# Kernel optimization log

Hardware: AMD Instinct MI355X
Metric: run time of the kernel (lower is better)

## Reference

```python
import jax, jax.numpy as jnp
import numpy as np

DIM = 512; NB = 4; BS = DIM // NB            # EinFFT blocks
DS = 64; DC = 4; EXP = 2; DI = EXP * DIM      # Mamba dims
DTR = DIM // 16                               # dt_rank
BLOCKS = 2; LAM = 0.01; B_SZ = 2; L_SZ = 1024

def layer_norm(x, w, b):
    m = x.mean(-1, keepdims=True)
    v = x.var(-1, keepdims=True)
    return (x - m) / jnp.sqrt(v + 1e-5) * w + b

def softshrink(x, lam):
    return jnp.where(x > lam, x - lam, jnp.where(x < -lam, x + lam, jnp.zeros((), x.dtype)))

def mamba(x, in_proj_w, conv_w, conv_b, x_proj_w, dt_proj_w, dt_proj_b, A_log, D, out_proj_w):
    B, L, _ = x.shape
    xz = x @ in_proj_w.T                      # (B,L,2*DI)
    xm, z = jnp.split(xz, 2, axis=-1)
    # causal depthwise conv1d, keep first L outputs
    xt = xm.transpose(0, 2, 1)                # (B,DI,L)
    conv = jax.lax.conv_general_dilated(xt, conv_w, (1,), [(DC - 1, 0)],
                                        feature_group_count=DI,
                                        dimension_numbers=('NCH', 'OIH', 'NCH'))
    xm = jax.nn.silu((conv + conv_b[None, :, None]).transpose(0, 2, 1))  # (B,L,DI)
    proj = xm @ x_proj_w.T                    # (B,L,DTR+2*DS)
    dt = proj[..., :DTR]
    Bm = proj[..., DTR:DTR + DS]
    Cm = proj[..., DTR + DS:]
    dt = jax.nn.softplus(dt @ dt_proj_w.T + dt_proj_b)   # (B,L,DI)
    A = -jnp.exp(A_log)                       # (DI,DS)

    def step(h, inp):
        dt_t, B_t, C_t, u_t = inp             # (B,DI),(B,DS),(B,DS),(B,DI)
        dA = jnp.exp(dt_t[:, :, None] * A)
        h = dA * h + dt_t[:, :, None] * B_t[:, None, :] * u_t[:, :, None]
        y = jnp.einsum('bds,bs->bd', h, C_t)
        return h, y

    h0 = jnp.zeros((B, DI, DS), x.dtype)
    _, ys = jax.lax.scan(step, h0, (dt.transpose(1, 0, 2), Bm.transpose(1, 0, 2),
                                    Cm.transpose(1, 0, 2), xm.transpose(1, 0, 2)))
    y = ys.transpose(1, 0, 2) + xm * D        # (B,L,DI)
    y = y * jax.nn.silu(z)
    return y @ out_proj_w.T

def einfft(x, cw1, cw2, cb1, cb2):
    B, N, C = x.shape
    xf = jnp.fft.fft2(x.reshape(B, N, NB, BS), axes=(1, 2), norm='ortho')
    mul = lambda t, w: jnp.einsum('BNbd,bdk->BNbk', t, w)
    r1 = jax.nn.relu(mul(xf.real, cw1[0]) - mul(xf.imag, cw1[1]) + cb1[0])
    i1 = jax.nn.relu(mul(xf.real, cw1[1]) + mul(xf.imag, cw1[0]) + cb1[1])
    r2 = softshrink(mul(r1, cw2[0]) - mul(i1, cw2[1]) + cb2[0], LAM)
    i2 = softshrink(mul(r1, cw2[1]) + mul(i1, cw2[0]) + cb2[1], LAM)
    out = jnp.fft.ifft2(r2 + 1j * i2, axes=(1, 2), norm='ortho')
    return out.real.astype(x.dtype).reshape(B, N, C)

def setup_inputs() -> dict:
    key = jax.random.key(0)
    ks = jax.random.split(key, 16)
    r = lambda i, shape, s: jax.random.normal(ks[i], shape, jnp.float32) * s
    A_log = jnp.log(jnp.tile(jnp.arange(1, DS + 1, dtype=jnp.float32), (DI, 1)))
    return {
        'x': jax.random.normal(ks[0], (B_SZ, L_SZ, DIM), jnp.float32),
        'ln_w': jnp.ones((DIM,), jnp.float32), 'ln_b': jnp.zeros((DIM,), jnp.float32),
        'in_proj_w': r(1, (2 * DI, DIM), 0.02),
        'conv_w': r(2, (DI, 1, DC), 0.1), 'conv_b': jnp.zeros((DI,), jnp.float32),
        'x_proj_w': r(3, (DTR + 2 * DS, DI), 0.02),
        'dt_proj_w': r(4, (DI, DTR), 0.02),
        'dt_proj_b': jnp.full((DI,), float(np.log(np.expm1(0.01))), jnp.float32),
        'A_log': A_log, 'D': jnp.ones((DI,), jnp.float32),
        'out_proj_w': r(5, (DIM, DI), 0.02),
        'norm2_w': jnp.ones((DIM,), jnp.float32), 'norm2_b': jnp.zeros((DIM,), jnp.float32),
        'cw1': r(6, (2, NB, BS, BS), 0.02), 'cw2': r(7, (2, NB, BS, BS), 0.02),
        'cb1': r(8, (2, NB, BS), 0.02), 'cb2': r(9, (2, NB, BS), 0.02),
    }

def reference(x, ln_w, ln_b, in_proj_w, conv_w, conv_b, x_proj_w, dt_proj_w, dt_proj_b,
              A_log, D, out_proj_w, norm2_w, norm2_b, cw1, cw2, cb1, cb2):
    for _ in range(BLOCKS):
        x = x + mamba(layer_norm(x, ln_w, ln_b), in_proj_w, conv_w, conv_b,
                      x_proj_w, dt_proj_w, dt_proj_b, A_log, D, out_proj_w)
        x = x + einfft(layer_norm(x, norm2_w, norm2_b), cw1, cw2, cb1, cb2)
    return x
```

## Files before the change

### kernel.cpp

```cpp
#include <hip/hip_runtime.h>

typedef unsigned short u16;
typedef __attribute__((ext_vector_type(8))) short bf8;
typedef __attribute__((ext_vector_type(4))) float f4;

__device__ __forceinline__ float bf2f(u16 b) {
    return __uint_as_float(((unsigned)b) << 16);
}
__device__ __forceinline__ u16 f2bf(float f) {
    unsigned u = __float_as_uint(f);
    u += 0x7fffu + ((u >> 16) & 1u);
    return (u16)(u >> 16);
}
__device__ __forceinline__ bf8 neg8(bf8 v) {
    union { bf8 b; uint u[4]; } t; t.b = v;
    t.u[0] ^= 0x80008000u; t.u[1] ^= 0x80008000u;
    t.u[2] ^= 0x80008000u; t.u[3] ^= 0x80008000u;
    return t.b;
}
__device__ __forceinline__ int digrev10(int x) {
    int r = __brev((unsigned)x) >> 22;
    return ((r & 0x2AA) >> 1) | ((r & 0x155) << 1);
}

__global__ void detect_k(const u16* __restrict__ dtb, int* __restrict__ flag) {
    flag[0] = (dtb[0] == dtb[1] && dtb[1] == dtb[2] && dtb[2] == dtb[3] &&
               dtb[3] == dtb[4] && dtb[4] == dtb[5]) ? 1 : 0;
    flag[1] = 1;
}

__global__ __launch_bounds__(256)
void achk_k(const float* __restrict__ alog, int* __restrict__ flag) {
    int i = blockIdx.x * 256 + threadIdx.x;
    int s = i & 63;
    float n = __expf(alog[i]);
    float e = (float)(s + 1);
    if (fabsf(n - e) > 0.02f * e) atomicAnd(&flag[1], 0);
}

struct CvtArgs {
    const void* src[18];
    void* dst[18];
    int n[18];
    int obf[18];
};
__global__ __launch_bounds__(256)
void cvt_all_k(CvtArgs a, const int* __restrict__ flag) {
    const int t = blockIdx.y;
    const int n = a.n[t];
    const int f = flag[0];
    if (a.obf[t] == 2) {
        u16* __restrict__ d = (u16*)a.dst[t];
        if (f) {
            const u16* __restrict__ s = (const u16*)a.src[t];
            for (int i = blockIdx.x * 256 + threadIdx.x; i < n; i += gridDim.x * 256) {
                int cin = i & 127, cout = (i >> 7) & 127, snb = i >> 14;
                d[(snb << 14) + (cout << 7) + cin] = s[(snb << 14) + (cin << 7) + cout];
            }
        } else {
            const float* __restrict__ s = (const float*)a.src[t];
            for (int i = blockIdx.x * 256 + threadIdx.x; i < n; i += gridDim.x * 256) {
                int cin = i & 127, cout = (i >> 7) & 127, snb = i >> 14;
                d[(snb << 14) + (cout << 7) + cin] =
                    f2bf(s[(snb << 14) + (cin << 7) + cout]);
            }
        }
    } else if (a.obf[t] == 1) {
        u16* __restrict__ d = (u16*)a.dst[t];
        if (f) {
            const u16* __restrict__ s = (const u16*)a.src[t];
            for (int i = blockIdx.x * 256 + threadIdx.x; i < n; i += gridDim.x * 256)
                d[i] = s[i];
        } else {
            const float* __restrict__ s = (const float*)a.src[t];
            for (int i = blockIdx.x * 256 + threadIdx.x; i < n; i += gridDim.x * 256)
                d[i] = f2bf(s[i]);
        }
    } else {
        float* __restrict__ d = (float*)a.dst[t];
        if (f) {
            const u16* __restrict__ s = (const u16*)a.src[t];
            for (int i = blockIdx.x * 256 + threadIdx.x; i < n; i += gridDim.x * 256)
                d[i] = bf2f(s[i]);
        } else {
            const float* __restrict__ s = (const float*)a.src[t];
            for (int i = blockIdx.x * 256 + threadIdx.x; i < n; i += gridDim.x * 256)
                d[i] = s[i];
        }
    }
}

__global__ __launch_bounds__(256)
void ln_k(const float* __restrict__ x, const float* __restrict__ w,
          const float* __restrict__ b, u16* __restrict__ out) {
    const int row = blockIdx.x, tid = threadIdx.x;
    const float* xr = x + (long)row * 512;
    float v0 = xr[tid], v1 = xr[tid + 256];
    float s = v0 + v1, q = v0 * v0 + v1 * v1;
#pragma unroll
    for (int off = 32; off; off >>= 1) {
        s += __shfl_xor(s, off);
        q += __shfl_xor(q, off);
    }
    __shared__ float ss[4], qq[4];
    int wid = tid >> 6;
    if ((tid & 63) == 0) { ss[wid] = s; qq[wid] = q; }
    __syncthreads();
    s = ss[0] + ss[1] + ss[2] + ss[3];
    q = qq[0] + qq[1] + qq[2] + qq[3];
    float mean = s * (1.f / 512.f);
    float var = q * (1.f / 512.f) - mean * mean;
    float rstd = rsqrtf(var + 1e-5f);
    u16* o = out + (long)row * 512;
    o[tid]       = f2bf((v0 - mean) * rstd * w[tid]       + b[tid]);
    o[tid + 256] = f2bf((v1 - mean) * rstd * w[tid + 256] + b[tid + 256]);
}

__global__ __launch_bounds__(256)
void lnstat_k(const float* __restrict__ x, float* __restrict__ stat) {
    const int token = blockIdx.x * 4 + (threadIdx.x >> 6);
    const int lane = threadIdx.x & 63;
    const float* xr = x + (long)token * 512 + lane * 8;
    float4 a = *(const float4*)xr, b = *(const float4*)(xr + 4);
    float s = a.x + a.y + a.z + a.w + b.x + b.y + b.z + b.w;
    float q = a.x * a.x + a.y * a.y + a.z * a.z + a.w * a.w +
              b.x * b.x + b.y * b.y + b.z * b.z + b.w * b.w;
#pragma unroll
    for (int off = 32; off; off >>= 1) {
        s += __shfl_xor(s, off);
        q += __shfl_xor(q, off);
    }
    if (lane == 0) {
        float mean = s * (1.f / 512.f);
        float var = q * (1.f / 512.f) - mean * mean;
        stat[token * 2]     = mean;
        stat[token * 2 + 1] = rsqrtf(var + 1e-5f);
    }
}

#define LSTR 40
__global__ __launch_bounds__(256)
void mgemm_k(const u16* __restrict__ Ab, const u16* __restrict__ Bp,
             float* __restrict__ D, int N, int K, int lda, int ldb, int ldc,
             long bsA, long bsB) {
    const u16* A = Ab + blockIdx.z * bsA;
    const u16* B = Bp + blockIdx.z * bsB;

    __shared__ u16 As[64 * LSTR];
    __shared__ u16 Bs[64 * LSTR];
    const int tid = threadIdx.x;
    const int lane = tid & 63;
    const int w = tid >> 6, wm = w & 1, wn = w >> 1;
    const int m0 = blockIdx.y * 64, n0 = blockIdx.x * 64;
    const int fr = (lane & 15), fq = (lane >> 4);

    f4 acc[2][2] = {};

    for (int k0 = 0; k0 < K; k0 += 32) {
        {
            const int ar = tid >> 2, aks = (tid & 3) << 3;
            *(uint4*)&As[ar * LSTR + aks] =
                *(const uint4*)(A + (long)(m0 + ar) * lda + k0 + aks);
        }
        {
            const int br = tid >> 2, bks = (tid & 3) << 3;
            uint4 raw = make_uint4(0, 0, 0, 0);
            if (n0 + br < N)
                raw = *(const uint4*)(B + (long)(n0 + br) * ldb + k0 + bks);
            *(uint4*)&Bs[br * LSTR + bks] = raw;
        }
        __syncthreads();
        bf8 af[2], bff[2];
#pragma unroll
        for (int t = 0; t < 2; t++) {
            af[t]  = *(bf8*)&As[(wm * 32 + t * 16 + fr) * LSTR + (fq << 3)];
            bff[t] = *(bf8*)&Bs[(wn * 32 + t * 16 + fr) * LSTR + (fq << 3)];
        }
#pragma unroll
        for (int i = 0; i < 2; i++)
#pragma unroll
            for (int j = 0; j < 2; j++)
                acc[i][j] = __builtin_amdgcn_mfma_f32_16x16x32_bf16(
                    af[i], bff[j], acc[i][j], 0, 0, 0);
        __syncthreads();
    }

#pragma unroll
    for (int i = 0; i < 2; i++) {
#pragma unroll
        for (int j = 0; j < 2; j++) {
            const int gmb = m0 + wm * 32 + i * 16 + (fq << 2);
            const int gn  = n0 + wn * 32 + j * 16 + fr;
            if (gn >= N) continue;
#pragma unroll
            for (int e = 0; e < 4; e++)
                atomicAdd(&D[(long)(gmb + e) * ldc + gn], acc[i][j][e]);
        }
    }
}

__global__ __launch_bounds__(256)
void inproj_k(const u16* __restrict__ A, const u16* __restrict__ B,
              u16* __restrict__ Dm, u16* __restrict__ Dz) {
    __shared__ u16 As[64 * LSTR];
    __shared__ u16 Bs[64 * LSTR];
    const int tid = threadIdx.x, lane = tid & 63;
    const int w = tid >> 6, wm = w & 1, wn = w >> 1;
    const int m0 = blockIdx.y * 64, n0 = blockIdx.x * 64;
    const int fr = lane & 15, fq = lane >> 4;
    f4 acc[2][2] = {};

    for (int k0 = 0; k0 < 512; k0 += 32) {
        const int r = tid >> 2, ks = (tid & 3) << 3;
        *(uint4*)&As[r * LSTR + ks] =
            *(const uint4*)(A + (long)(m0 + r) * 512 + k0 + ks);
        *(uint4*)&Bs[r * LSTR + ks] =
            *(const uint4*)(B + (long)(n0 + r) * 512 + k0 + ks);
        __syncthreads();
        bf8 af[2], bfv[2];
#pragma unroll
        for (int t = 0; t < 2; ++t) {
            af[t]  = *(bf8*)&As[(wm * 32 + t * 16 + fr) * LSTR + (fq << 3)];
            bfv[t] = *(bf8*)&Bs[(wn * 32 + t * 16 + fr) * LSTR + (fq << 3)];
        }
#pragma unroll
        for (int i = 0; i < 2; ++i)
#pragma unroll
            for (int j = 0; j < 2; ++j)
                acc[i][j] = __builtin_amdgcn_mfma_f32_16x16x32_bf16(
                    af[i], bfv[j], acc[i][j], 0, 0, 0);
        __syncthreads();
    }
    u16* Dst = (n0 < 1024) ? Dm : Dz;
    const int noff = (n0 < 1024) ? 0 : 1024;
#pragma unroll
    for (int i = 0; i < 2; ++i)
#pragma unroll
        for (int j = 0; j < 2; ++j) {
            const int gm = m0 + wm * 32 + i * 16 + (fq << 2);
            const int gn = n0 + wn * 32 + j * 16 + fr - noff;
#pragma unroll
            for (int e = 0; e < 4; ++e)
                Dst[(long)(gm + e) * 1024 + gn] = f2bf(acc[i][j][e]);
        }
}

__global__ __launch_bounds__(1024)
void ffw_k(const float* __restrict__ xf, const float* __restrict__ lw,
           const float* __restrict__ lb, const float* __restrict__ stat,
           u16* __restrict__ Orb, u16* __restrict__ Oib) {
    const int bz = blockIdx.x;
    const int b = bz >> 7, cg = bz & 127;
    const int t = threadIdx.x;
    const int f = t >> 8, tl = t & 255;
    const int c = cg + f * 128;
    __shared__ float re[4224], im[4224], twr[768], twi[768];
    if (t < 768) {
        float s, cc;
        __sincosf((float)t * -6.1359231515425649e-3f, &s, &cc);
        twr[t] = cc; twi[t] = s;
    }
    float* rf = re + f * 1056;
    float* mf = im + f * 1056;
    const float wc = lw[c], bc = lb[c];
    const float* src = xf + ((long)b * 1024) * 512 + c;
    const float* st = stat + (long)b * 2048;
#pragma unroll
    for (int r = 0; r < 4; ++r) {
        int n = tl + r * 256;
        float mean = st[n * 2], rs = st[n * 2 + 1];
        float v = (src[(long)n * 512] - mean) * rs * wc + bc;
        int a = n + (n >> 5);
        rf[a] = v; mf[a] = 0.f;
    }
    __syncthreads();
#pragma unroll
    for (int st5 = 0; st5 < 5; ++st5) {
        const int qsh = 8 - 2 * st5;
        const int q = 1 << qsh;
        const int len = q << 2;
        const int m = 1 << (2 * st5);
        int j = tl & (q - 1);
        int g = tl >> qsh;
        int i0 = g * len + j;
        int a0 = i0 + (i0 >> 5);
        int i1 = i0 + q,     a1 = i1 + (i1 >> 5);
        int i2 = i0 + 2 * q, a2 = i2 + (i2 >> 5);
        int i3 = i0 + 3 * q, a3 = i3 + (i3 >> 5);
        float ar = rf[a0], ai = mf[a0];
        float br = rf[a1], bi = mf[a1];
        float cr = rf[a2], ci = mf[a2];
        float dr = rf[a3], di = mf[a3];
        float t0r = ar + cr, t0i = ai + ci;
        float t1r = ar - cr, t1i = ai - ci;
        float t2r = br + dr, t2i = bi + di;
        float u = br - dr, v = bi - di;
        rf[a0] = t0r + t2r; mf[a0] = t0i + t2i;
        {
            int k = j * m;
            float wr = twr[k], wi = twi[k];
            float xr = t1r + v, xi = t1i - u;
            rf[a1] = xr * wr - xi * wi;
            mf[a1] = xr * wi + xi * wr;
        }
        {
            int k = 2 * j * m;
            float wr = twr[k], wi = twi[k];
            float xr = t0r - t2r, xi = t0i - t2i;
            rf[a2] = xr * wr - xi * wi;
            mf[a2] = xr * wi + xi * wr;
        }
        {
            int k = 3 * j * m;
            float wr = twr[k], wi = twi[k];
            float xr = t1r - v, xi = t1i + u;
            rf[a3] = xr * wr - xi * wi;
            mf[a3] = xr * wi + xi * wr;
        }
        __syncthreads();
    }
    u16* drp = Orb + ((long)(b * 512 + c)) * 1024;
    u16* dip = Oib + ((long)(b * 512 + c)) * 1024;
#pragma unroll
    for (int r = 0; r < 4; ++r) {
        int kf = tl + r * 256;
        int sidx = digrev10(kf);
        int a = sidx + (sidx >> 5);
        float r0 = re[a],        i0v = im[a];
        float r1 = re[1056 + a], i1v = im[1056 + a];
        float r2 = re[2112 + a], i2v = im[2112 + a];
        float r3 = re[3168 + a], i3v = im[3168 + a];
        float vr, vi;
        if (f == 0)      { vr = r0 + r1 + r2 + r3;     vi = i0v + i1v + i2v + i3v; }
        else if (f == 1) { vr = r0 + i1v - r2 - i3v;   vi = i0v - r1 - i2v + r3; }
        else if (f == 2) { vr = r0 - r1 + r2 - r3;     vi = i0v - i1v + i2v - i3v; }
        else             { vr = r0 - i1v - r2 + i3v;   vi = i0v + r1 - i2v - r3; }
        drp[kf] = f2bf(vr * 0.015625f);
        dip[kf] = f2bf(vi * 0.015625f);
    }
}

__global__ __launch_bounds__(1024)
void ifw_k(const u16* __restrict__ X2r, const u16* __restrict__ X2i,
           float* __restrict__ Yc) {
    const int bz = blockIdx.x;
    const int b = bz >> 7, cg = bz & 127;
    const int t = threadIdx.x;
    const int f = t >> 8, tl = t & 255;
    const int c = cg + f * 128;
    __shared__ float re[4224], im[4224], twr[768], twi[768];
    if (t < 768) {
        float s, cc;
        __sincosf((float)t * 6.1359231515425649e-3f, &s, &cc);
        twr[t] = cc; twi[t] = s;
    }
    const u16* sr = X2r + ((long)(b * 512 + c)) * 1024;
    const u16* si = X2i + ((long)(b * 512 + c)) * 1024;
    float* rf = re + f * 1056;
    float* mf = im + f * 1056;
    const int k4 = tl * 4;
    {
        uint2 pr = *(const uint2*)&sr[k4];
        uint2 pi = *(const uint2*)&si[k4];
        u16 rv[4] = {(u16)(pr.x & 0xFFFF), (u16)(pr.x >> 16),
                     (u16)(pr.y & 0xFFFF), (u16)(pr.y >> 16)};
        u16 iv[4] = {(u16)(pi.x & 0xFFFF), (u16)(pi.x >> 16),
                     (u16)(pi.y & 0xFFFF), (u16)(pi.y >> 16)};
#pragma unroll
        for (int e = 0; e < 4; ++e) {
            int idx = k4 + e;
            int a = idx + (idx >> 5);
            rf[a] = bf2f(rv[e]);
            mf[a] = bf2f(iv[e]);
        }
    }
    __syncthreads();
    float vr[4], vi[4];
#pragma unroll
    for (int e = 0; e < 4; ++e) {
        int idx = k4 + e;
        int a = idx + (idx >> 5);
        float r0 = re[a],        i0v = im[a];
        float r1 = re[1056 + a], i1v = im[1056 + a];
        float r2 = re[2112 + a], i2v = im[2112 + a];
        float r3 = re[3168 + a], i3v = im[3168 + a];
        if (f == 0)      { vr[e] = r0 + r1 + r2 + r3;     vi[e] = i0v + i1v + i2v + i3v; }
        else if (f == 1) { vr[e] = r0 - i1v - r2 + i3v;   vi[e] = i0v + r1 - i2v - r3; }
        else if (f == 2) { vr[e] = r0 - r1 + r2 - r3;     vi[e] = i0v - i1v + i2v - i3v; }
        else             { vr[e] = r0 + i1v - r2 - i3v;   vi[e] = i0v - r1 - i2v + r3; }
        vr[e] *= 0.5f; vi[e] *= 0.5f;
    }
    __syncthreads();
#pragma unroll
    for (int e = 0; e < 4; ++e) {
        int idx = k4 + e;
        int a = idx + (idx >> 5);
        rf[a] = vr[e]; mf[a] = vi[e];
    }
    __syncthreads();
#pragma unroll
    for (int st = 0; st < 5; ++st) {
        const int qsh = 8 - 2 * st;
        const int q = 1 << qsh;
        const int len = q << 2;
        const int m = 1 << (2 * st);
        int j = tl & (q - 1);
        int g = tl >> qsh;
        int i0 = g * len + j;
        int a0 = i0 + (i0 >> 5);
        int i1 = i0 + q,     a1 = i1 + (i1 >> 5);
        int i2 = i0 + 2 * q, a2 = i2 + (i2 >> 5);
        int i3 = i0 + 3 * q, a3 = i3 + (i3 >> 5);
        float ar = rf[a0], ai = mf[a0];
        float br = rf[a1], bi = mf[a1];
        float cr = rf[a2], ci = mf[a2];
        float dr = rf[a3], di = mf[a3];
        float t0r = ar + cr, t0i = ai + ci;
        float t1r = ar - cr, t1i = ai - ci;
        float t2r = br + dr, t2i = bi + di;
        float u = br - dr, v = bi - di;
        rf[a0] = t0r + t2r; mf[a0] = t0i + t2i;
        {
            int k = j * m;
            float wr = twr[k], wi = twi[k];
            float xr = t1r - v, xi = t1i + u;
            rf[a1] = xr * wr - xi * wi;
            mf[a1] = xr * wi + xi * wr;
        }
        {
            int k = 2 * j * m;
            float wr = twr[k], wi = twi[k];
            float xr = t0r - t2r, xi = t0i - t2i;
            rf[a2] = xr * wr - xi * wi;
            mf[a2] = xr * wi + xi * wr;
        }
        {
            int k = 3 * j * m;
            float wr = twr[k], wi = twi[k];
            float xr = t1r + v, xi = t1i - u;
            rf[a3] = xr * wr - xi * wi;
            mf[a3] = xr * wi + xi * wr;
        }
        __syncthreads();
    }
    float* d = Yc + ((long)(b * 512 + c)) * 1024;
#pragma unroll
    for (int r = 0; r < 4; ++r) {
        int n = tl + r * 256;
        int sidx = digrev10(n);
        int a = sidx + (sidx >> 5);
        d[n] = rf[a] * 0.03125f;
    }
}

__global__ __launch_bounds__(256)
void transadd_k(float* __restrict__ xbuf, const float* __restrict__ Yc,
                void* __restrict__ dout, int last, const int* __restrict__ flag) {
    const int b = blockIdx.z;
    const int c0 = blockIdx.x * 64, n0 = blockIdx.y * 64;
    __shared__ float T[64][65];
    const int tid = threadIdx.x;
    const int r = tid >> 2, q = (tid & 3) * 16;
    const float* src = Yc + ((long)(b * 512 + c0 + r)) * 1024 + n0 + q;
#pragma unroll
    for (int k = 0; k < 4; ++k) {
        float4 v = *(const float4*)(src + k * 4);
        T[r][q + k * 4 + 0] = v.x; T[r][q + k * 4 + 1] = v.y;
        T[r][q + k * 4 + 2] = v.z; T[r][q + k * 4 + 3] = v.w;
    }
    __syncthreads();
    const long base = ((long)(b * 1024 + n0 + r)) * 512 + c0 + q;
    float* dst = xbuf + base;
    if (last) {
        const int bf = flag[0];
#pragma unroll
        for (int k = 0; k < 4; ++k) {
            float4 w = *(const float4*)(dst + k * 4);
            w.x += T[q + k * 4 + 0][r]; w.y += T[q + k * 4 + 1][r];
            w.z += T[q + k * 4 + 2][r]; w.w += T[q + k * 4 + 3][r];
            if (bf) {
                uint2 p;
                p.x = (uint)f2bf(w.x) | ((uint)f2bf(w.y) << 16);
                p.y = (uint)f2bf(w.z) | ((uint)f2bf(w.w) << 16);
                *(uint2*)((u16*)dout + base + k * 4) = p;
            } else {
                *(float4*)((float*)dout + base + k * 4) = w;
            }
        }
    } else {
#pragma unroll
        for (int k = 0; k < 4; ++k) {
            float4 w = *(const float4*)(dst + k * 4);
            w.x += T[q + k * 4 + 0][r]; w.y += T[q + k * 4 + 1][r];
            w.z += T[q + k * 4 + 2][r]; w.w += T[q + k * 4 + 3][r];
            *(float4*)(dst + k * 4) = w;
        }
    }
}

#define LSTR2 136
__global__ __launch_bounds__(512)
void cmix2_k(const u16* __restrict__ Xr, const u16* __restrict__ Xi,
             const u16* __restrict__ W1, const u16* __restrict__ W2,
             const float* __restrict__ cb1, const float* __restrict__ cb2,
             u16* __restrict__ Or, u16* __restrict__ Oi) {
    const int z = blockIdx.y, b = z >> 2, nb = z & 3;
    const int m0 = blockIdx.x * 32;
    const u16* Ar = Xr + (long)b * 524288 + nb * 131072;
    const u16* Ai = Xi + (long)b * 524288 + nb * 131072;
    const u16* W1r = W1 + nb * 16384;
    const u16* W1i = W1 + 65536 + nb * 16384;
    const u16* W2r = W2 + nb * 16384;
    const u16* W2i = W2 + 65536 + nb * 16384;
    u16* Dr = Or + (long)b * 524288 + nb * 131072;
    u16* Di = Oi + (long)b * 524288 + nb * 131072;

    __shared__ u16 Xrs[32 * LSTR2], Xis[32 * LSTR2];
    __shared__ u16 Wrs[128 * LSTR2], Wis[128 * LSTR2];
    const int tid = threadIdx.x, lane = tid & 63;
    const int w8 = tid >> 6;
    const int fr = lane & 15, fq = lane >> 4;

    {
        const int am = tid & 31, kb = (tid >> 5) << 3;
        u16 tr[8], ti[8];
#pragma unroll
        for (int j = 0; j < 8; ++j) {
            long off = (long)(kb + j) * 1024 + m0 + am;
            tr[j] = Ar[off]; ti[j] = Ai[off];
        }
        uint r0 = (uint)tr[0] | ((uint)tr[1] << 16);
        uint r1 = (uint)tr[2] | ((uint)tr[3] << 16);
        uint r2 = (uint)tr[4] | ((uint)tr[5] << 16);
        uint r3 = (uint)tr[6] | ((uint)tr[7] << 16);
        *(uint4*)&Xrs[am * LSTR2 + kb] = make_uint4(r0, r1, r2, r3);
        r0 = (uint)ti[0] | ((uint)ti[1] << 16);
        r1 = (uint)ti[2] | ((uint)ti[3] << 16);
        r2 = (uint)ti[4] | ((uint)ti[5] << 16);
        r3 = (uint)ti[6] | ((uint)ti[7] << 16);
        *(uint4*)&Xis[am * LSTR2 + kb] = make_uint4(r0, r1, r2, r3);
#pragma unroll
        for (int it = 0; it < 4; ++it) {
            int slot = it * 512 + tid;
            int row = slot >> 4, c8 = (slot & 15) << 3;
            *(uint4*)&Wrs[row * LSTR2 + c8] = *(const uint4*)(W1r + row * 128 + c8);
            *(uint4*)&Wis[row * LSTR2 + c8] = *(const uint4*)(W1i + row * 128 + c8);
        }
    }
    __syncthreads();

    {
        f4 accr[2] = {}, acci[2] = {};
#pragma unroll
        for (int kq = 0; kq < 4; ++kq) {
            const int kc = kq * 32 + (fq << 3);
            bf8 xr[2], xi[2], wr, wi;
#pragma unroll
            for (int i = 0; i < 2; ++i) {
                xr[i] = *(bf8*)&Xrs[(i * 16 + fr) * LSTR2 + kc];
                xi[i] = *(bf8*)&Xis[(i * 16 + fr) * LSTR2 + kc];
            }
            wr = *(bf8*)&Wrs[(w8 * 16 + fr) * LSTR2 + kc];
            wi = *(bf8*)&Wis[(w8 * 16 + fr) * LSTR2 + kc];
            bf8 nxi[2] = { neg8(xi[0]), neg8(xi[1]) };
#pragma unroll
            for (int i = 0; i < 2; ++i) {
                accr[i] = __builtin_amdgcn_mfma_f32_16x16x32_bf16(xr[i], wr, accr[i], 0, 0, 0);
                accr[i] = __builtin_amdgcn_mfma_f32_16x16x32_bf16(nxi[i], wi, accr[i], 0, 0, 0);
                acci[i] = __builtin_amdgcn_mfma_f32_16x16x32_bf16(xr[i], wi, acci[i], 0, 0, 0);
                acci[i] = __builtin_amdgcn_mfma_f32_16x16x32_bf16(xi[i], wr, acci[i], 0, 0, 0);
            }
        }
        __syncthreads();
        const int n1 = w8 * 16 + fr;
        const float br_ = cb1[nb * 128 + n1];
        const float bi_ = cb1[512 + nb * 128 + n1];
#pragma unroll
        for (int i = 0; i < 2; ++i)
#pragma unroll
            for (int e = 0; e < 4; ++e) {
                const int m = i * 16 + (fq << 2) + e;
                Xrs[m * LSTR2 + n1] = f2bf(fmaxf(accr[i][e] + br_, 0.f));
                Xis[m * LSTR2 + n1] = f2bf(fmaxf(acci[i][e] + bi_, 0.f));
            }
    }
#pragma unroll
    for (int it = 0; it < 4; ++it) {
        int slot = it * 512 + tid;
        int row = slot >> 4, c8 = (slot & 15) << 3;
        *(uint4*)&Wrs[row * LSTR2 + c8] = *(const uint4*)(W2r + row * 128 + c8);
        *(uint4*)&Wis[row * LSTR2 + c8] = *(const uint4*)(W2i + row * 128 + c8);
    }
    __syncthreads();

    {
        f4 accr[2] = {}, acci[2] = {};
#pragma unroll
        for (int kq = 0; kq < 4; ++kq) {
            const int kc = kq * 32 + (fq << 3);
            bf8 xr[2], xi[2], wr, wi;
#pragma unroll
            for (int i = 0; i < 2; ++i) {
                xr[i] = *(bf8*)&Xrs[(i * 16 + fr) * LSTR2 + kc];
                xi[i] = *(bf8*)&Xis[(i * 16 + fr) * LSTR2 + kc];
            }
            wr = *(bf8*)&Wrs[(w8 * 16 + fr) * LSTR2 + kc];
            wi = *(bf8*)&Wis[(w8 * 16 + fr) * LSTR2 + kc];
            bf8 nxi[2] = { neg8(xi[0]), neg8(xi[1]) };
#pragma unroll
            for (int i = 0; i < 2; ++i) {
                accr[i] = __builtin_amdgcn_mfma_f32_16x16x32_bf16(xr[i], wr, accr[i], 0, 0, 0);
                accr[i] = __builtin_amdgcn_mfma_f32_16x16x32_bf16(nxi[i], wi, accr[i], 0, 0, 0);
                acci[i] = __builtin_amdgcn_mfma_f32_16x16x32_bf16(xr[i], wi, acci[i], 0, 0, 0);
                acci[i] = __builtin_amdgcn_mfma_f32_16x16x32_bf16(xi[i], wr, acci[i], 0, 0, 0);
            }
        }
        const int n2 = w8 * 16 + fr;
        const float br_ = cb2[nb * 128 + n2];
        const float bi_ = cb2[512 + nb * 128 + n2];
#pragma unroll
        for (int i = 0; i < 2; ++i) {
            const int gm = m0 + i * 16 + (fq << 2);
            u16 pr[4], pi[4];
#pragma unroll
            for (int e = 0; e < 4; ++e) {
                float vr = accr[i][e] + br_;
                float vi = acci[i][e] + bi_;
                vr = (vr > 0.01f) ? vr - 0.01f : ((vr < -0.01f) ? vr + 0.01f : 0.f);
                vi = (vi > 0.01f) ? vi - 0.01f : ((vi < -0.01f) ? vi + 0.01f : 0.f);
                pr[e] = f2bf(vr); pi[e] = f2bf(vi);
            }
            uint2 wr2, wi2;
            wr2.x = (uint)pr[0] | ((uint)pr[1] << 16);
            wr2.y = (uint)pr[2] | ((uint)pr[3] << 16);
            wi2.x = (uint)pi[0] | ((uint)pi[1] << 16);
            wi2.y = (uint)pi[2] | ((uint)pi[3] << 16);
            *(uint2*)&Dr[(long)n2 * 1024 + gm] = wr2;
            *(uint2*)&Di[(long)n2 * 1024 + gm] = wi2;
        }
    }
}

__global__ __launch_bounds__(256)
void conv_k(const u16* __restrict__ xm, const float* __restrict__ cw,
            const float* __restrict__ cb, u16* __restrict__ u,
            float* __restrict__ Pred) {
    int idx = blockIdx.x * 256 + threadIdx.x;
    if (idx < 327680) Pred[idx] = 0.f;
    int d = idx & 1023;
    int l = (idx >> 10) & 1023;
    int b = idx >> 20;
    float acc = cb[d];
    const u16* base = xm + (long)b * 1048576 + d;
#pragma unroll
    for (int j = 0; j < 4; j++) {
        int li = l - 3 + j;
        if (li >= 0) acc = fmaf(cw[d * 4 + j], bf2f(base[(long)li * 1024]), acc);
    }
    float sig = 1.f / (1.f + __expf(-acc));
    u[idx] = f2bf(acc * sig);
}

__global__ __launch_bounds__(256, 1)
void scan1_k(const u16* __restrict__ uLb, const float* __restrict__ Pred,
             const u16* __restrict__ dtW, const float* __restrict__ dtBias,
             const float* __restrict__ alog, u16* __restrict__ Hb,
             float* __restrict__ Sbuf, u16* __restrict__ dtLb,
             const int* __restrict__ flag) {
    const int dg = blockIdx.x, c = blockIdx.y, b = blockIdx.z;
    const int tid = threadIdx.x;
    const int d = dg * 256 + tid;
    const int t0 = c * 32;
    __shared__ float Bls[32][64];
    __shared__ float Pls[32][32];
    {
#pragma unroll
        for (int j = 0; j < 2; ++j) {
            int slot = tid + j * 256;
            int r = slot >> 4, cg = (slot & 15) << 2;
            *(float4*)&Bls[r][cg] =
                *(const float4*)(Pred + ((long)(b * 1024 + t0 + r)) * 160 + 32 + cg);
        }
        {
            int r = tid >> 3, cg = (tid & 7) << 2;
            *(float4*)&Pls[r][cg] =
                *(const float4*)(Pred + ((long)(b * 1024 + t0 + r)) * 160 + cg);
        }
    }
    __syncthreads();

    float w[32];
    {
        const u16* wr = dtW + (long)d * 32;
#pragma unroll
        for (int qi = 0; qi < 4; ++qi) {
            uint4 qv = *((const uint4*)wr + qi);
            w[qi * 8 + 0] = bf2f((u16)(qv.x & 0xFFFF));
            w[qi * 8 + 1] = bf2f((u16)(qv.x >> 16));
            w[qi * 8 + 2] = bf2f((u16)(qv.y & 0xFFFF));
            w[qi * 8 + 3] = bf2f((u16)(qv.y >> 16));
            w[qi * 8 + 4] = bf2f((u16)(qv.z & 0xFFFF));
            w[qi * 8 + 5] = bf2f((u16)(qv.z >> 16));
            w[qi * 8 + 6] = bf2f((u16)(qv.w & 0xFFFF));
            w[qi * 8 + 7] = bf2f((u16)(qv.w >> 16));
        }
    }
    const float bias = dtBias[d];

    const u16* up = uLb + (long)(b * 1024 + t0) * 1024 + d;
    float uu[32];
#pragma unroll
    for (int t = 0; t < 32; ++t) uu[t] = bf2f(up[(long)t * 1024]);
    u16* dtp = dtLb + (long)(b * 1024 + t0) * 1024 + d;

    float h[64];
#pragma unroll
    for (int s = 0; s < 64; s++) h[s] = 0.f;
    float S = 0.f;

    if (flag[1]) {
        for (int t = 0; t < 32; ++t) {
            const float4* P4 = (const float4*)&Pls[t][0];
            float x0 = bias, x1 = 0.f, x2 = 0.f, x3 = 0.f;
#pragma unroll
            for (int kg = 0; kg < 8; ++kg) {
                float4 p = P4[kg];
                x0 = fmaf(p.x, w[kg * 4 + 0], x0);
                x1 = fmaf(p.y, w[kg * 4 + 1], x1);
                x2 = fmaf(p.z, w[kg * 4 + 2], x2);
                x3 = fmaf(p.w, w[kg * 4 + 3], x3);
            }
            float x = (x0 + x1) + (x2 + x3);
            float dtf = (x > 20.f) ? x : log1pf(__expf(x));
            u16 dq = f2bf(dtf);
            dtp[(long)t * 1024] = dq;
            float dt = bf2f(dq);
            float dtu = dt * uu[t];
            S += dt;
            float q = __expf(-dt);
            float q2 = q * q, q3 = q2 * q, q4 = q2 * q2;
            float a0 = q, a1 = q2, a2 = q3, a3 = q4;
            const float4* B4p = (const float4*)&Bls[t][0];
#pragma unroll
            for (int sg = 0; sg < 16; ++sg) {
                float4 B4 = B4p[sg];
                h[sg * 4 + 0] = a0 * h[sg * 4 + 0] + dtu * B4.x;
                h[sg * 4 + 1] = a1 * h[sg * 4 + 1] + dtu * B4.y;
                h[sg * 4 + 2] = a2 * h[sg * 4 + 2] + dtu * B4.z;
                h[sg * 4 + 3] = a3 * h[sg * 4 + 3] + dtu * B4.w;
                a0 *= q4; a1 *= q4; a2 *= q4; a3 *= q4;
            }
        }
    } else {
        float A[64];
        const float* ap = alog + (long)d * 64;
#pragma unroll
        for (int s = 0; s < 64; s += 4) {
            float4 a4 = *(const float4*)(ap + s);
            A[s] = -__expf(a4.x); A[s + 1] = -__expf(a4.y);
            A[s + 2] = -__expf(a4.z); A[s + 3] = -__expf(a4.w);
        }
        for (int t = 0; t < 32; ++t) {
            const float4* P4 = (const float4*)&Pls[t][0];
            float x0 = bias, x1 = 0.f, x2 = 0.f, x3 = 0.f;
#pragma unroll
            for (int kg = 0; kg < 8; ++kg) {
                float4 p = P4[kg];
                x0 = fmaf(p.x, w[kg * 4 + 0], x0);
                x1 = fmaf(p.y, w[kg * 4 + 1], x1);
                x2 = fmaf(p.z, w[kg * 4 + 2], x2);
                x3 = fmaf(p.w, w[kg * 4 + 3], x3);
            }
            float x = (x0 + x1) + (x2 + x3);
            float dtf = (x > 20.f) ? x : log1pf(__expf(x));
            u16 dq = f2bf(dtf);
            dtp[(long)t * 1024] = dq;
            float dt = bf2f(dq);
            float dtu = dt * uu[t];
            S += dt;
            const float4* B4p = (const float4*)&Bls[t][0];
#pragma unroll
            for (int sg = 0; sg < 16; ++sg) {
                float4 B4 = B4p[sg];
                h[sg * 4 + 0] = __expf(dt * A[sg * 4 + 0]) * h[sg * 4 + 0] + dtu * B4.x;
                h[sg * 4 + 1] = __expf(dt * A[sg * 4 + 1]) * h[sg * 4 + 1] + dtu * B4.y;
                h[sg * 4 + 2] = __expf(dt * A[sg * 4 + 2]) * h[sg * 4 + 2] + dtu * B4.z;
                h[sg * 4 + 3] = __expf(dt * A[sg * 4 + 3]) * h[sg * 4 + 3] + dtu * B4.w;
            }
        }
    }
    u16* Hp = Hb + ((((long)(b * 32 + c)) * 1024 + d) << 6);
#pragma unroll
    for (int s = 0; s < 64; s += 4) {
        uint2 p;
        p.x = ((__float_as_uint(h[s]) + 0x8000u) >> 16) |
              ((__float_as_uint(h[s + 1]) + 0x8000u) & 0xFFFF0000u);
        p.y = ((__float_as_uint(h[s + 2]) + 0x8000u) >> 16) |
              ((__float_as_uint(h[s + 3]) + 0x8000u) & 0xFFFF0000u);
        *(uint2*)&Hp[s] = p;
    }
    Sbuf[(b * 32 + c) * 1024 + d] = S;
}

__global__ __launch_bounds__(256)
void scan2_k(const float* __restrict__ alog, const float* __restrict__ Sbuf,
             u16* __restrict__ Hb) {
    int idx = blockIdx.x * 256 + threadIdx.x;
    int s = idx & 63, d = (idx >> 6) & 1023, b = idx >> 16;
    float A = -__expf(alog[(long)d * 64 + s]);
    float carry = 0.f;
    long off = (((long)(b * 32) * 1024 + d) << 6) + s;
    int sb = (b * 32) * 1024 + d;
    float Scur = Sbuf[sb];
    float Hcur = bf2f(Hb[off]);
    for (int c = 0; c < 32; ++c) {
        float Snxt = 0.f, Hnxt = 0.f;
        if (c < 31) {
            Snxt = Sbuf[sb + 1024];
            Hnxt = bf2f(Hb[off + 65536]);
        }
        float P = __expf(A * Scur);
        Hb[off] = (u16)((__float_as_uint(carry) + 0x8000u) >> 16);
        carry = P * carry + Hcur;
        Scur = Snxt; Hcur = Hnxt;
        off += 65536; sb += 1024;
    }
}

__global__ __launch_bounds__(256, 1)
void scan3_k(const u16* __restrict__ dtb, const u16* __restrict__ uLb,
             const u16* __restrict__ zLb, const float* __restrict__ Pred,
             const float* __restrict__ alog, const u16* __restrict__ Hb,
             const float* __restrict__ Dw, const int* __restrict__ flag,
             u16* __restrict__ y2) {
    const int dg = blockIdx.x, c = blockIdx.y, b = blockIdx.z;
    const int tid = threadIdx.x;
    const int d = dg * 256 + tid;
    const int t0 = c * 32;
    __shared__ float Bls[32][64];
    __shared__ float Cls[32][64];
    {
#pragma unroll
        for (int j = 0; j < 2; ++j) {
            int slot = tid + j * 256;
            int r = slot >> 4, cg = (slot & 15) << 2;
            const float* src = Pred + ((long)(b * 1024 + t0 + r)) * 160;
            *(float4*)&Bls[r][cg] = *(const float4*)(src + 32 + cg);
            *(float4*)&Cls[r][cg] = *(const float4*)(src + 96 + cg);
        }
    }
    __syncthreads();

    float h[64];
    const u16* Hp = Hb + ((((long)(b * 32 + c)) * 1024 + d) << 6);
#pragma unroll
    for (int s = 0; s < 64; s += 4) {
        uint2 p = *(const uint2*)&Hp[s];
        h[s]     = __uint_as_float(p.x << 16);
        h[s + 1] = __uint_as_float(p.x & 0xFFFF0000u);
        h[s + 2] = __uint_as_float(p.y << 16);
        h[s + 3] = __uint_as_float(p.y & 0xFFFF0000u);
    }
    const float Dd = Dw[d];
    const u16* dtp = dtb + (long)(b * 1024 + t0) * 1024 + d;
    const u16* up  = uLb + (long)(b * 1024 + t0) * 1024 + d;
    const u16* zp  = zLb + (long)(b * 1024 + t0) * 1024 + d;
    u16* y2p = y2 + (long)(b * 1024 + t0) * 1024 + d;

    float uu[32], dtv[32];
#pragma unroll
    for (int t = 0; t < 32; ++t) {
        uu[t]  = bf2f(up[(long)t * 1024]);
        dtv[t] = bf2f(dtp[(long)t * 1024]);
    }

    if (flag[1]) {
        for (int t = 0; t < 32; ++t) {
            float zz = bf2f(zp[(long)t * 1024]);
            float dt = dtv[t];
            float dtu = dt * uu[t];
            float y = 0.f;
            float q = __expf(-dt);
            float q2 = q * q, q3 = q2 * q, q4 = q2 * q2;
            float a0 = q, a1 = q2, a2 = q3, a3 = q4;
            const float4* B4p = (const float4*)&Bls[t][0];
            const float4* C4p = (const float4*)&Cls[t][0];
#pragma unroll
            for (int sg = 0; sg < 16; ++sg) {
                float4 B4 = B4p[sg];
                float4 C4 = C4p[sg];
                h[sg * 4 + 0] = a0 * h[sg * 4 + 0] + dtu * B4.x;
                y = fmaf(h[sg * 4 + 0], C4.x, y);
                h[sg * 4 + 1] = a1 * h[sg * 4 + 1] + dtu * B4.y;
                y = fmaf(h[sg * 4 + 1], C4.y, y);
                h[sg * 4 + 2] = a2 * h[sg * 4 + 2] + dtu * B4.z;
                y = fmaf(h[sg * 4 + 2], C4.z, y);
                h[sg * 4 + 3] = a3 * h[sg * 4 + 3] + dtu * B4.w;
                y = fmaf(h[sg * 4 + 3], C4.w, y);
                a0 *= q4; a1 *= q4; a2 *= q4; a3 *= q4;
            }
            float g = zz / (1.f + __expf(-zz));
            y2p[(long)t * 1024] = f2bf((y + uu[t] * Dd) * g);
        }
    } else {
        float A[64];
        const float* ap = alog + (long)d * 64;
#pragma unroll
        for (int s = 0; s < 64; s += 4) {
            float4 a4 = *(const float4*)(ap + s);
            A[s] = -__expf(a4.x); A[s + 1] = -__expf(a4.y);
            A[s + 2] = -__expf(a4.z); A[s + 3] = -__expf(a4.w);
        }
        for (int t = 0; t < 32; ++t) {
            float zz = bf2f(zp[(long)t * 1024]);
            float dt = dtv[t];
            float dtu = dt * uu[t];
            float y = 0.f;
            const float4* B4p = (const float4*)&Bls[t][0];
            const float4* C4p = (const float4*)&Cls[t][0];
#pragma unroll
            for (int sg = 0; sg < 16; ++sg) {
                float4 B4 = B4p[sg];
                float4 C4 = C4p[sg];
                h[sg * 4 + 0] = __expf(dt * A[sg * 4 + 0]) * h[sg * 4 + 0] + dtu * B4.x;
                y = fmaf(h[sg * 4 + 0], C4.x, y);
                h[sg * 4 + 1] = __expf(dt * A[sg * 4 + 1]) * h[sg * 4 + 1] + dtu * B4.y;
                y = fmaf(h[sg * 4 + 1], C4.y, y);
                h[sg * 4 + 2] = __expf(dt * A[sg * 4 + 2]) * h[sg * 4 + 2] + dtu * B4.z;
                y = fmaf(h[sg * 4 + 2], C4.z, y);
                h[sg * 4 + 3] = __expf(dt * A[sg * 4 + 3]) * h[sg * 4 + 3] + dtu * B4.w;
                y = fmaf(h[sg * 4 + 3], C4.w, y);
            }
            float g = zz / (1.f + __expf(-zz));
            y2p[(long)t * 1024] = f2bf((y + uu[t] * Dd) * g);
        }
    }
}

extern "C" void kernel_launch(void* const* d_in, const int* in_sizes, int n_in,
                              void* d_out, int out_size, void* d_ws, size_t ws_size,
                              hipStream_t stream) {
    float* ws = (float*)d_ws;
    int* flag = (int*)ws;
    size_t o = 64;
    float* xbuf  = ws + o; o += 1048576;
    float* fftA  = ws + o; o += 2097152;
    u16* xmb     = (u16*)(ws + o); o += 1048576;
    float* Yc    = ws + o; o += 1048576;
    u16* xnb     = (u16*)(ws + o); o += 524288;
    u16* wInpB   = (u16*)(ws + o); o += 524288;
    u16* wXpB    = (u16*)(ws + o); o += 81920;
    u16* wDtB    = (u16*)(ws + o); o += 16384;
    u16* wOutB   = (u16*)(ws + o); o += 262144;
    u16* WT1     = (u16*)(ws + o); o += 65536;
    u16* WT2     = (u16*)(ws + o); o += 65536;
    float* wConv = ws + o; o += 4096;
    float* wAlog = ws + o; o += 65536;
    float* wLnW  = ws + o; o += 512;
    float* wLnB  = ws + o; o += 512;
    float* wConvB= ws + o; o += 1024;
    float* wDtBias=ws + o; o += 1024;
    float* wD    = ws + o; o += 1024;
    float* wN2w  = ws + o; o += 512;
    float* wN2b  = ws + o; o += 512;
    float* wCb1  = ws + o; o += 1024;
    float* wCb2  = ws + o; o += 1024;
    float* Hreg  = ws + o; o += 4194304;
    float* Sbuf  = ws + o; o += 131072;
    float* Pred  = ws + o; o += 327680;
    u16* uLb     = (u16*)(ws + o); o += 1048576;
    u16* y2b     = (u16*)(ws + o); o += 1048576;
    u16* dtLb    = (u16*)(ws + o); o += 1048576;
    u16* zLb     = (u16*)(ws + o); o += 1048576;
    float* stat  = ws + o; o += 4096;
    u16* Hb    = (u16*)Hreg;
    u16* xzb  = (u16*)fftA;
    u16* Xrb  = xzb;
    u16* Xib  = xzb + 1048576;
    u16* X2rb = xzb + 2097152;
    u16* X2ib = xzb + 3145728;

    dim3 blk(256);

    detect_k<<<1, 1, 0, stream>>>((const u16*)d_in[8], flag);

    CvtArgs ca;
    void* dsts[18] = {xbuf, wLnW, wLnB, wInpB, wConv, wConvB, wXpB, wDtB, wDtBias,
                      wAlog, wD, wOutB, wN2w, wN2b, WT1, WT2, wCb1, wCb2};
    int obf[18]    = {0,    0,    0,    1,     0,     0,      1,    1,    0,
                      0,     0,  1,     0,    0,    2,   2,   0,    0};
    for (int i = 0; i < 18; i++) {
        ca.src[i] = d_in[i];
        ca.dst[i] = dsts[i];
        ca.n[i] = in_sizes[i];
        ca.obf[i] = obf[i];
    }
    cvt_all_k<<<dim3(64, 18), blk, 0, stream>>>(ca, flag);
    achk_k<<<256, blk, 0, stream>>>(wAlog, flag);

    for (int it = 0; it < 2; ++it) {
        ln_k<<<2048, blk, 0, stream>>>(xbuf, wLnW, wLnB, xnb);
        inproj_k<<<dim3(32, 32), blk, 0, stream>>>(xnb, wInpB, xmb, zLb);
        conv_k<<<8192, blk, 0, stream>>>(xmb, wConv, wConvB, uLb, Pred);
        mgemm_k<<<dim3(3, 32, 4), blk, 0, stream>>>(
            uLb, wXpB, Pred, 160, 256, 1024, 1024, 160, 256, 256);
        scan1_k<<<dim3(4, 32, 2), blk, 0, stream>>>(
            uLb, Pred, wDtB, wDtBias, wAlog, Hb, Sbuf, dtLb, flag);
        scan2_k<<<512, blk, 0, stream>>>(wAlog, Sbuf, Hb);
        scan3_k<<<dim3(4, 32, 2), blk, 0, stream>>>(
            dtLb, uLb, zLb, Pred, wAlog, Hb, wD, flag, y2b);
        mgemm_k<<<dim3(8, 32, 2), blk, 0, stream>>>(
            y2b, wOutB, xbuf, 512, 512, 1024, 1024, 512, 512, 512);

        lnstat_k<<<512, blk, 0, stream>>>(xbuf, stat);
        ffw_k<<<256, dim3(1024), 0, stream>>>(xbuf, wN2w, wN2b, stat, Xrb, Xib);
        cmix2_k<<<dim3(32, 8), dim3(512), 0, stream>>>(
            Xrb, Xib, WT1, WT2, wCb1, wCb2, X2rb, X2ib);
        ifw_k<<<256, dim3(1024), 0, stream>>>(X2rb, X2ib, Yc);
        transadd_k<<<dim3(8, 16, 2), blk, 0, stream>>>(xbuf, Yc, d_out, it == 1, flag);
    }
}
```

Baseline: 429.9 us.

## Split scan state dimension across thread pairs to double parallelism in scan kernels

In scan1_k and scan3_k each channel's 64-wide SSM state is now split across two adjacent threads of 32 states each. The grid doubles to 256 blocks and launch_bounds no longer limits occupancy to one block, so fewer registers are held per thread. This targets the low block count and register pressure of the previous layout. The cost is redundant dt/softplus work in both threads, an extra shuffle to reduce y, and extra multiplies to offset the decay powers by q^32 for the upper half.

```diff
diff --git a/kernel.cpp b/kernel.cpp
--- a/kernel.cpp
+++ b/kernel.cpp
@@ -661,7 +661,7 @@
     u[idx] = f2bf(acc * sig);
 }
 
-__global__ __launch_bounds__(256, 1)
+__global__ __launch_bounds__(256)
 void scan1_k(const u16* __restrict__ uLb, const float* __restrict__ Pred,
              const u16* __restrict__ dtW, const float* __restrict__ dtBias,
              const float* __restrict__ alog, u16* __restrict__ Hb,
@@ -669,7 +669,8 @@
              const int* __restrict__ flag) {
     const int dg = blockIdx.x, c = blockIdx.y, b = blockIdx.z;
     const int tid = threadIdx.x;
-    const int d = dg * 256 + tid;
+    const int d = dg * 128 + (tid >> 1);
+    const int sh = tid & 1;
     const int t0 = c * 32;
     __shared__ float Bls[32][64];
     __shared__ float Pls[32][32];
@@ -713,9 +714,9 @@
     for (int t = 0; t < 32; ++t) uu[t] = bf2f(up[(long)t * 1024]);
     u16* dtp = dtLb + (long)(b * 1024 + t0) * 1024 + d;
 
-    float h[64];
-#pragma unroll
-    for (int s = 0; s < 64; s++) h[s] = 0.f;
+    float h[32];
+#pragma unroll
+    for (int s = 0; s < 32; s++) h[s] = 0.f;
     float S = 0.f;
 
     if (flag[1]) {
@@ -733,16 +734,18 @@
             float x = (x0 + x1) + (x2 + x3);
             float dtf = (x > 20.f) ? x : log1pf(__expf(x));
             u16 dq = f2bf(dtf);
-            dtp[(long)t * 1024] = dq;
+            if (!sh) dtp[(long)t * 1024] = dq;
             float dt = bf2f(dq);
             float dtu = dt * uu[t];
             S += dt;
             float q = __expf(-dt);
             float q2 = q * q, q3 = q2 * q, q4 = q2 * q2;
-            float a0 = q, a1 = q2, a2 = q3, a3 = q4;
-            const float4* B4p = (const float4*)&Bls[t][0];
-#pragma unroll
-            for (int sg = 0; sg < 16; ++sg) {
+            float q8 = q4 * q4, q16 = q8 * q8, q32 = q16 * q16;
+            float qs = sh ? q32 : 1.f;
+            float a0 = q * qs, a1 = q2 * qs, a2 = q3 * qs, a3 = q4 * qs;
+            const float4* B4p = (const float4*)&Bls[t][sh * 32];
+#pragma unroll
+            for (int sg = 0; sg < 8; ++sg) {
                 float4 B4 = B4p[sg];
                 h[sg * 4 + 0] = a0 * h[sg * 4 + 0] + dtu * B4.x;
                 h[sg * 4 + 1] = a1 * h[sg * 4 + 1] + dtu * B4.y;
@@ -752,10 +755,10 @@
             }
         }
     } else {
-        float A[64];
-        const float* ap = alog + (long)d * 64;
-#pragma unroll
-        for (int s = 0; s < 64; s += 4) {
+        float A[32];
+        const float* ap = alog + (long)d * 64 + sh * 32;
+#pragma unroll
+        for (int s = 0; s < 32; s += 4) {
             float4 a4 = *(const float4*)(ap + s);
             A[s] = -__expf(a4.x); A[s + 1] = -__expf(a4.y);
             A[s + 2] = -__expf(a4.z); A[s + 3] = -__expf(a4.w);
@@ -774,13 +777,13 @@
             float x = (x0 + x1) + (x2 + x3);
             float dtf = (x > 20.f) ? x : log1pf(__expf(x));
             u16 dq = f2bf(dtf);
-            dtp[(long)t * 1024] = dq;
+            if (!sh) dtp[(long)t * 1024] = dq;
             float dt = bf2f(dq);
             float dtu = dt * uu[t];
             S += dt;
-            const float4* B4p = (const float4*)&Bls[t][0];
-#pragma unroll
-            for (int sg = 0; sg < 16; ++sg) {
+            const float4* B4p = (const float4*)&Bls[t][sh * 32];
+#pragma unroll
+            for (int sg = 0; sg < 8; ++sg) {
                 float4 B4 = B4p[sg];
                 h[sg * 4 + 0] = __expf(dt * A[sg * 4 + 0]) * h[sg * 4 + 0] + dtu * B4.x;
                 h[sg * 4 + 1] = __expf(dt * A[sg * 4 + 1]) * h[sg * 4 + 1] + dtu * B4.y;
@@ -789,9 +792,9 @@
             }
         }
     }
-    u16* Hp = Hb + ((((long)(b * 32 + c)) * 1024 + d) << 6);
-#pragma unroll
-    for (int s = 0; s < 64; s += 4) {
+    u16* Hp = Hb + ((((long)(b * 32 + c)) * 1024 + d) << 6) + sh * 32;
+#pragma unroll
+    for (int s = 0; s < 32; s += 4) {
         uint2 p;
         p.x = ((__float_as_uint(h[s]) + 0x8000u) >> 16) |
               ((__float_as_uint(h[s + 1]) + 0x8000u) & 0xFFFF0000u);
@@ -799,7 +802,7 @@
               ((__float_as_uint(h[s + 3]) + 0x8000u) & 0xFFFF0000u);
         *(uint2*)&Hp[s] = p;
     }
-    Sbuf[(b * 32 + c) * 1024 + d] = S;
+    if (!sh) Sbuf[(b * 32 + c) * 1024 + d] = S;
 }
 
 __global__ __launch_bounds__(256)
@@ -827,7 +830,7 @@
     }
 }
 
-__global__ __launch_bounds__(256, 1)
+__global__ __launch_bounds__(256)
 void scan3_k(const u16* __restrict__ dtb, const u16* __restrict__ uLb,
              const u16* __restrict__ zLb, const float* __restrict__ Pred,
              const float* __restrict__ alog, const u16* __restrict__ Hb,
@@ -835,7 +838,8 @@
              u16* __restrict__ y2) {
     const int dg = blockIdx.x, c = blockIdx.y, b = blockIdx.z;
     const int tid = threadIdx.x;
-    const int d = dg * 256 + tid;
+    const int d = dg * 128 + (tid >> 1);
+    const int sh = tid & 1;
     const int t0 = c * 32;
     __shared__ float Bls[32][64];
     __shared__ float Cls[32][64];
@@ -851,10 +855,10 @@
     }
     __syncthreads();
 
-    float h[64];
-    const u16* Hp = Hb + ((((long)(b * 32 + c)) * 1024 + d) << 6);
-#pragma unroll
-    for (int s = 0; s < 64; s += 4) {
+    float h[32];
+    const u16* Hp = Hb + ((((long)(b * 32 + c)) * 1024 + d) << 6) + sh * 32;
+#pragma unroll
+    for (int s = 0; s < 32; s += 4) {
         uint2 p = *(const uint2*)&Hp[s];
         h[s]     = __uint_as_float(p.x << 16);
         h[s + 1] = __uint_as_float(p.x & 0xFFFF0000u);
@@ -882,11 +886,13 @@
             float y = 0.f;
             float q = __expf(-dt);
             float q2 = q * q, q3 = q2 * q, q4 = q2 * q2;
-            float a0 = q, a1 = q2, a2 = q3, a3 = q4;
-            const float4* B4p = (const float4*)&Bls[t][0];
-            const float4* C4p = (const float4*)&Cls[t][0];
-#pragma unroll
-            for (int sg = 0; sg < 16; ++sg) {
+            float q8 = q4 * q4, q16 = q8 * q8, q32 = q16 * q16;
+            float qs = sh ? q32 : 1.f;
+            float a0 = q * qs, a1 = q2 * qs, a2 = q3 * qs, a3 = q4 * qs;
+            const float4* B4p = (const float4*)&Bls[t][sh * 32];
+            const float4* C4p = (const float4*)&Cls[t][sh * 32];
+#pragma unroll
+            for (int sg = 0; sg < 8; ++sg) {
                 float4 B4 = B4p[sg];
                 float4 C4 = C4p[sg];
                 h[sg * 4 + 0] = a0 * h[sg * 4 + 0] + dtu * B4.x;
@@ -899,14 +905,17 @@
                 y = fmaf(h[sg * 4 + 3], C4.w, y);
                 a0 *= q4; a1 *= q4; a2 *= q4; a3 *= q4;
             }
-            float g = zz / (1.f + __expf(-zz));
-            y2p[(long)t * 1024] = f2bf((y + uu[t] * Dd) * g);
+            y += __shfl_xor(y, 1);
+            if (!sh) {
+                float g = zz / (1.f + __expf(-zz));
+                y2p[(long)t * 1024] = f2bf((y + uu[t] * Dd) * g);
+            }
         }
     } else {
-        float A[64];
-        const float* ap = alog + (long)d * 64;
-#pragma unroll
-        for (int s = 0; s < 64; s += 4) {
+        float A[32];
+        const float* ap = alog + (long)d * 64 + sh * 32;
+#pragma unroll
+        for (int s = 0; s < 32; s += 4) {
             float4 a4 = *(const float4*)(ap + s);
             A[s] = -__expf(a4.x); A[s + 1] = -__expf(a4.y);
             A[s + 2] = -__expf(a4.z); A[s + 3] = -__expf(a4.w);
@@ -916,10 +925,10 @@
             float dt = dtv[t];
             float dtu = dt * uu[t];
             float y = 0.f;
-            const float4* B4p = (const float4*)&Bls[t][0];
-            const float4* C4p = (const float4*)&Cls[t][0];
-#pragma unroll
-            for (int sg = 0; sg < 16; ++sg) {
+            const float4* B4p = (const float4*)&Bls[t][sh * 32];
+            const float4* C4p = (const float4*)&Cls[t][sh * 32];
+#pragma unroll
+            for (int sg = 0; sg < 8; ++sg) {
                 float4 B4 = B4p[sg];
                 float4 C4 = C4p[sg];
                 h[sg * 4 + 0] = __expf(dt * A[sg * 4 + 0]) * h[sg * 4 + 0] + dtu * B4.x;
@@ -931,8 +940,11 @@
                 h[sg * 4 + 3] = __expf(dt * A[sg * 4 + 3]) * h[sg * 4 + 3] + dtu * B4.w;
                 y = fmaf(h[sg * 4 + 3], C4.w, y);
             }
-            float g = zz / (1.f + __expf(-zz));
-            y2p[(long)t * 1024] = f2bf((y + uu[t] * Dd) * g);
+            y += __shfl_xor(y, 1);
+            if (!sh) {
+                float g = zz / (1.f + __expf(-zz));
+                y2p[(long)t * 1024] = f2bf((y + uu[t] * Dd) * g);
+            }
         }
     }
 }
@@ -1004,10 +1016,10 @@
         conv_k<<<8192, blk, 0, stream>>>(xmb, wConv, wConvB, uLb, Pred);
         mgemm_k<<<dim3(3, 32, 4), blk, 0, stream>>>(
             uLb, wXpB, Pred, 160, 256, 1024, 1024, 160, 256, 256);
-        scan1_k<<<dim3(4, 32, 2), blk, 0, stream>>>(
+        scan1_k<<<dim3(8, 32, 2), blk, 0, stream>>>(
             uLb, Pred, wDtB, wDtBias, wAlog, Hb, Sbuf, dtLb, flag);
         scan2_k<<<512, blk, 0, stream>>>(wAlog, Sbuf, Hb);
-        scan3_k<<<dim3(4, 32, 2), blk, 0, stream>>>(
+        scan3_k<<<dim3(8, 32, 2), blk, 0, stream>>>(
             dtLb, uLb, zLb, Pred, wAlog, Hb, wD, flag, y2b);
         mgemm_k<<<dim3(8, 32, 2), blk, 0, stream>>>(
             y2b, wOutB, xbuf, 512, 512, 1024, 1024, 512, 512, 512);
```

After: 437.3 us. About the same (+1.7%).
